# Kernel optimization log

Hardware: AMD Instinct MI355X
Metric: run time of the kernel (lower is better)

Reference implementation:

```python
import jax, jax.numpy as jnp
import numpy as np

B, T, I = 8, 8192, 512
E, K, J = 16, 1024, 512

def setup_inputs() -> dict:
    key = jax.random.key(0)
    k1, k2, k3 = jax.random.split(key, 3)
    x = jax.random.normal(k1, (B, T, I), dtype=jnp.float32)
    Ind = jax.random.randint(k2, (B, E, K), 0, T, dtype=jnp.int32)
    bound = 1.0 / np.sqrt(I)
    W = jax.random.uniform(k3, (E, I, J), dtype=jnp.float32, minval=-bound, maxval=bound)
    return {"x": x, "Ind": Ind, "W": W}

def reference(x, Ind, W):
    # gather: [B,E,K,I] = x[b, Ind[b,e,k], :]
    gathered = jnp.take_along_axis(x[:, None, :, :], Ind[:, :, :, None], axis=2)
    # per-expert GEMM: [B,E,K,J]
    return jnp.einsum('beki,eij->bekj', gathered, W)
```

## Files before the change

### kernel.cpp

```cpp
#include <hip/hip_runtime.h>
#include <stdint.h>

typedef short short8 __attribute__((ext_vector_type(8)));
typedef float floatx16 __attribute__((ext_vector_type(16)));

constexpr int CB = 8;
constexpr int CT = 8192;
constexpr int CI = 512;
constexpr int CE = 16;
constexpr int CK = 1024;
constexpr int CJ = 512;

__device__ uint32_t g_xb[(size_t)CB * CT * CI / 2];
__device__ uint32_t g_wb[(size_t)CE * CI * CJ / 2];

__device__ __forceinline__ uint32_t f2bf(float f) {
    union { float f; uint32_t u; } c; c.f = f;
    return (c.u + 0x7fffu + ((c.u >> 16) & 1u)) >> 16;
}
__device__ __forceinline__ uint32_t pack2(float lo, float hi) {
    return f2bf(lo) | (f2bf(hi) << 16);
}

__device__ __forceinline__ void gl_lds16(const uint32_t* g, uint32_t* l) {
    __builtin_amdgcn_global_load_lds(
        (const __attribute__((address_space(1))) uint32_t*)g,
        (__attribute__((address_space(3))) uint32_t*)l,
        16, 0, 0);
}

constexpr int XBLK = CB * CT * CI / 8 / 256;
constexpr int WBLK = CE * CI * CJ / 8 / 256;
__global__ __launch_bounds__(256) void cvt_xw(
    const float* __restrict__ x, uint32_t* __restrict__ xb,
    const float* __restrict__ W, uint32_t* __restrict__ wb)
{
    const int bid = blockIdx.x;
    if (bid < XBLK) {
        size_t i = (size_t)bid * 256 + threadIdx.x;
        const float4* src = (const float4*)x;
        float4 a = src[2 * i], b = src[2 * i + 1];
        ((uint4*)xb)[i] = make_uint4(pack2(a.x, a.y), pack2(a.z, a.w),
                                     pack2(b.x, b.y), pack2(b.z, b.w));
    } else {
        uint32_t tid = (uint32_t)(bid - XBLK) * 256 + threadIdx.x;
        int jn  = tid & 127;
        int kpq = (tid >> 7) & 7;
        int kt  = (tid >> 10) & 7;
        int nt  = (tid >> 13) & 3;
        int e   = tid >> 15;
        int n   = nt * 128 + jn;
        int k0  = kt * 64 + kpq * 8;
        const float* src = W + ((size_t)e * CI + k0) * CJ + n;
        uint4 o;
        o.x = pack2(src[0 * CJ], src[1 * CJ]);
        o.y = pack2(src[2 * CJ], src[3 * CJ]);
        o.z = pack2(src[4 * CJ], src[5 * CJ]);
        o.w = pack2(src[6 * CJ], src[7 * CJ]);
        ((uint4*)wb)[tid] = o;
    }
}

__device__ __forceinline__ void stage_tiles(const uint32_t* const* pA, const uint32_t* pB,
                                            int kt, uint32_t* As, uint32_t* Bs, int wv) {
    #pragma unroll
    for (int i = 0; i < 4; ++i)
        gl_lds16(pA[i] + kt * 32, &As[wv * 1024 + i * 256]);
    #pragma unroll
    for (int i = 0; i < 4; ++i)
        gl_lds16(pB + (size_t)kt * 4096 + i * 256, &Bs[wv * 1024 + i * 256]);
}

__device__ __forceinline__ void compute_tile(const uint32_t* As, const uint32_t* Bs,
                                             int wm, int wn, int lrow, int lh,
                                             floatx16 acc[2][2]) {
    #pragma unroll
    for (int s = 0; s < 4; ++s) {
        short8 af[2], bfr[2];
        #pragma unroll
        for (int mt = 0; mt < 2; ++mt) {
            const int row = wm + mt * 32 + lrow;
            const int ch = (s * 2 + lh) ^ (lrow & 7);
            af[mt] = *(const short8*)&As[row * 32 + ch * 4];
        }
        #pragma unroll
        for (int nt = 0; nt < 2; ++nt) {
            const int jn = wn + nt * 32 + lrow;
            bfr[nt] = *(const short8*)&Bs[(s * 2 + lh) * 512 + jn * 4];
        }
        #pragma unroll
        for (int mt = 0; mt < 2; ++mt)
            #pragma unroll
            for (int nt = 0; nt < 2; ++nt)
                acc[mt][nt] = __builtin_amdgcn_mfma_f32_32x32x16_bf16(
                    af[mt], bfr[nt], acc[mt][nt], 0, 0, 0);
    }
}

__global__ __launch_bounds__(256, 2) void eg_kernel(
    const uint32_t* __restrict__ xb, const int* __restrict__ Ind,
    const uint32_t* __restrict__ wb, float* __restrict__ out)
{
    __shared__ __align__(16) uint32_t As0[128 * 32], As1[128 * 32];
    __shared__ __align__(16) uint32_t Bs0[32 * 128], Bs1[32 * 128];
    __shared__ int s_idx[128];

    const int t = threadIdx.x;
    const int z = blockIdx.z;
    const int e = z & (CE - 1);
    const int b = z >> 4;
    const int mtile = blockIdx.y;
    const int ntile = blockIdx.x;

    if (t < 128) s_idx[t] = Ind[z * CK + mtile * 128 + t];
    __syncthreads();

    const int ln = t & 63, wv = t >> 6;

    const int sr = ln >> 3;
    const int gchunk = (ln & 7) ^ sr;
    const uint32_t* xb_b = xb + (size_t)b * CT * 256;
    const uint32_t* pA[4];
    #pragma unroll
    for (int i = 0; i < 4; ++i) {
        int r = wv * 32 + i * 8 + sr;
        pA[i] = xb_b + (size_t)s_idx[r] * 256 + gchunk * 4;
    }
    const uint32_t* pB = wb + ((size_t)(e * 4 + ntile) * 8) * 4096 + wv * 1024 + ln * 4;

    const int wm = (wv >> 1) * 64, wn = (wv & 1) * 64;
    const int lrow = ln & 31;
    const int lh = ln >> 5;

    const floatx16 fz = {0.f,0.f,0.f,0.f,0.f,0.f,0.f,0.f,0.f,0.f,0.f,0.f,0.f,0.f,0.f,0.f};
    floatx16 acc[2][2] = {{fz, fz}, {fz, fz}};

    stage_tiles(pA, pB, 0, As0, Bs0, wv);
    __syncthreads();
    #pragma unroll
    for (int ktp = 0; ktp < 4; ++ktp) {
        stage_tiles(pA, pB, 2 * ktp + 1, As1, Bs1, wv);
        compute_tile(As0, Bs0, wm, wn, lrow, lh, acc);
        __syncthreads();
        if (ktp < 3)
            stage_tiles(pA, pB, 2 * ktp + 2, As0, Bs0, wv);
        compute_tile(As1, Bs1, wm, wn, lrow, lh, acc);
        __syncthreads();
    }

    const size_t obase = (size_t)z * CK * CJ;
    #pragma unroll
    for (int mt = 0; mt < 2; ++mt) {
        const int gm0 = mtile * 128 + wm + mt * 32 + lh * 4;
        #pragma unroll
        for (int nt = 0; nt < 2; ++nt) {
            const int gn = ntile * 128 + wn + nt * 32 + lrow;
            #pragma unroll
            for (int r = 0; r < 16; ++r) {
                const int gm = gm0 + (r & 3) + 8 * (r >> 2);
                out[obase + (size_t)gm * CJ + gn] = acc[mt][nt][r];
            }
        }
    }
}

extern "C" void kernel_launch(void* const* d_in, const int* in_sizes, int n_in,
                              void* d_out, int out_size, void* d_ws, size_t ws_size,
                              hipStream_t stream) {
    const float* x   = (const float*)d_in[0];
    const int*   Ind = (const int*)d_in[1];
    const float* W   = (const float*)d_in[2];
    float* out = (float*)d_out;

    uint32_t* xb; hipGetSymbolAddress((void**)&xb, HIP_SYMBOL(g_xb));
    uint32_t* wb; hipGetSymbolAddress((void**)&wb, HIP_SYMBOL(g_wb));

    hipLaunchKernelGGL(cvt_xw, dim3(XBLK + WBLK), dim3(256), 0, stream, x, xb, W, wb);

    dim3 grid(CJ / 128, CK / 128, CB * CE);
    hipLaunchKernelGGL(eg_kernel, grid, dim3(256), 0, stream, xb, Ind, wb, out);
}
```

Measured before the change: 473.5 us.

## Pipeline K-loop with partial vmcnt waits and remap blocks for XCD locality

Rewrites the double-buffered K loop so each iteration issues the next tile's global-to-LDS loads, then waits only for the older batch with s_waitcnt vmcnt(8) before a barrier. The aim is to keep one tile of loads in flight during compute instead of draining everything at each __syncthreads. It also flattens the grid to 1D and remaps block IDs so consecutive blocks landing on the same XCD share the same (b,e) tiles, improving L2 reuse of W and the gathered rows. Raw s_barrier with sched_barrier relies on manual waitcnt correctness, which is a risk if the compiler inserts extra memory ops.

```diff
diff --git a/kernel.cpp b/kernel.cpp
--- a/kernel.cpp
+++ b/kernel.cpp
@@ -97,6 +97,12 @@
     }
 }
 
+__device__ __forceinline__ void fence_barrier() {
+    __builtin_amdgcn_sched_barrier(0);
+    __builtin_amdgcn_s_barrier();
+    __builtin_amdgcn_sched_barrier(0);
+}
+
 __global__ __launch_bounds__(256, 2) void eg_kernel(
     const uint32_t* __restrict__ xb, const int* __restrict__ Ind,
     const uint32_t* __restrict__ wb, float* __restrict__ out)
@@ -106,11 +112,12 @@
     __shared__ int s_idx[128];
 
     const int t = threadIdx.x;
-    const int z = blockIdx.z;
+    const uint32_t id2 = (blockIdx.x & 7) * 512 + (blockIdx.x >> 3);
+    const int ntile = id2 & 3;
+    const int mtile = (id2 >> 2) & 7;
+    const int z = id2 >> 5;
     const int e = z & (CE - 1);
     const int b = z >> 4;
-    const int mtile = blockIdx.y;
-    const int ntile = blockIdx.x;
 
     if (t < 128) s_idx[t] = Ind[z * CK + mtile * 128 + t];
     __syncthreads();
@@ -136,16 +143,22 @@
     floatx16 acc[2][2] = {{fz, fz}, {fz, fz}};
 
     stage_tiles(pA, pB, 0, As0, Bs0, wv);
-    __syncthreads();
     #pragma unroll
-    for (int ktp = 0; ktp < 4; ++ktp) {
-        stage_tiles(pA, pB, 2 * ktp + 1, As1, Bs1, wv);
-        compute_tile(As0, Bs0, wm, wn, lrow, lh, acc);
-        __syncthreads();
-        if (ktp < 3)
-            stage_tiles(pA, pB, 2 * ktp + 2, As0, Bs0, wv);
-        compute_tile(As1, Bs1, wm, wn, lrow, lh, acc);
-        __syncthreads();
+    for (int kt = 0; kt < 8; ++kt) {
+        uint32_t* Acur = (kt & 1) ? As1 : As0;
+        uint32_t* Bcur = (kt & 1) ? Bs1 : Bs0;
+        uint32_t* Anxt = (kt & 1) ? As0 : As1;
+        uint32_t* Bnxt = (kt & 1) ? Bs0 : Bs1;
+        if (kt < 7) {
+            stage_tiles(pA, pB, kt + 1, Anxt, Bnxt, wv);
+            asm volatile("s_waitcnt vmcnt(8)" ::: "memory");
+        } else {
+            asm volatile("s_waitcnt vmcnt(0)" ::: "memory");
+        }
+        fence_barrier();
+        compute_tile(Acur, Bcur, wm, wn, lrow, lh, acc);
+        if (kt < 7)
+            fence_barrier();
     }
 
     const size_t obase = (size_t)z * CK * CJ;
@@ -177,6 +190,5 @@
 
     hipLaunchKernelGGL(cvt_xw, dim3(XBLK + WBLK), dim3(256), 0, stream, x, xb, W, wb);
 
-    dim3 grid(CJ / 128, CK / 128, CB * CE);
-    hipLaunchKernelGGL(eg_kernel, grid, dim3(256), 0, stream, xb, Ind, wb, out);
+    hipLaunchKernelGGL(eg_kernel, dim3(4096), dim3(256), 0, stream, xb, Ind, wb, out);
 }
```

After: 469.5 us. Within noise of the previous version (-0.8%).
